# Performance work log

Measured on AMD Instinct MI355X. Metric: run time of the kernel, lower is better.

## Reference

```python
import jax, jax.numpy as jnp
import numpy as np

# PyTorch LSTM cell with zero initial (h, c): W_hh @ h0 == 0, and c = sigmoid(i)*tanh(g)
# since the forget-gate term f*c0 vanishes. Gate order in torch: i, f, g, o.
# b here is the combined b_ih + b_hh (identical math).

def lstm_step0(x, Wih, b):
    pre = x @ Wih.T + b                      # (N, 4H)
    i, f, g, o = jnp.split(pre, 4, axis=-1)
    c = jax.nn.sigmoid(i) * jnp.tanh(g)
    return jax.nn.sigmoid(o) * jnp.tanh(c)   # (N, H)


def setup_inputs() -> dict:
    key = jax.random.key(0)
    ks = jax.random.split(key, 13)
    num_ts, num_periods, F = 128, 256, 128
    GH, NH, NF = 512, 256, 10
    s = lambda k, shape, fan: (jax.random.normal(k, shape, jnp.float32) / np.sqrt(fan))
    return {
        "X": jax.random.normal(ks[0], (num_ts, num_periods, F), jnp.float32),
        "g_Wih0": s(ks[1], (4 * GH, F), F),
        "g_b0": s(ks[2], (4 * GH,), GH),
        "g_Wih1": s(ks[3], (4 * GH, GH), GH),
        "g_b1": s(ks[4], (4 * GH,), GH),
        "aff_W": s(ks[5], (NF, GH), GH),
        "aff_b": s(ks[6], (NF,), GH),
        "n_Wih0": s(ks[7], (4 * NH, F), F),
        "n_b0": s(ks[8], (4 * NH,), NH),
        "n_Wih1": s(ks[9], (4 * NH, NH), NH),
        "n_b1": s(ks[10], (4 * NH,), NH),
        "noise_W": s(ks[11], (1, NH), NH),
        "noise_b": s(ks[12], (1,), NH),
    }


def reference(X, g_Wih0, g_b0, g_Wih1, g_b1, aff_W, aff_b,
              n_Wih0, n_b0, n_Wih1, n_b1, noise_W, noise_b):
    num_ts, num_periods, num_feats = X.shape
    x = X.reshape(-1, num_feats)             # (num_ts*num_periods, F)

    # Global factor branch: 2-layer LSTM single step from zero state
    hg = lstm_step0(lstm_step0(x, g_Wih0, g_b0), g_Wih1, g_b1)
    hg = jax.nn.relu(hg)
    mus = (hg @ aff_W.T + aff_b).sum(axis=-1).reshape(num_ts, num_periods)

    # Noise branch: 2-layer LSTM single step from zero state
    hn = lstm_step0(lstm_step0(x, n_Wih0, n_b0), n_Wih1, n_b1)
    hn = jax.nn.relu(hn)
    sigmas = jax.nn.softplus(hn @ noise_W.T + noise_b)  # log(1+exp(.)), stable
    sigmas = sigmas.reshape(num_ts, num_periods) + 1e-6
    return mus, sigmas
```

## Files before the change

### kernel.cpp

```cpp
#include <hip/hip_runtime.h>
#include <hip/hip_bf16.h>
#include <hip/hip_fp16.h>

typedef _Float16 h8_t __attribute__((ext_vector_type(8)));
typedef _Float16 h4_t __attribute__((ext_vector_type(4)));
typedef float f4_t __attribute__((ext_vector_type(4)));

#define M_ROWS 32768

__device__ __forceinline__ void gload_lds16(const void* g, void* l) {
  __builtin_amdgcn_global_load_lds((const __attribute__((address_space(1))) void*)g,
                                   (__attribute__((address_space(3))) void*)l, 16, 0, 0);
}

__device__ __forceinline__ float sigmoid_f(float x) { return 1.f / (1.f + __expf(-x)); }
__device__ __forceinline__ float tanh_f(float x) { return 1.f - 2.f / (__expf(2.f * x) + 1.f); }

struct GArgs {
  const _Float16* A;
  const _Float16* W;
  const float* bias;
  _Float16* Hout;
  const float* rvec;
  float* partial;
};

__global__ void prep_all(const float* __restrict__ X, const float* __restrict__ gW0,
                         const float* __restrict__ gW1, const float* __restrict__ nW0,
                         const float* __restrict__ nW1, const float* __restrict__ aff_W,
                         const float* __restrict__ aff_b,
                         _Float16* __restrict__ Xh, _Float16* __restrict__ Wg0,
                         _Float16* __restrict__ Wg1, _Float16* __restrict__ Wn0,
                         _Float16* __restrict__ Wn1,
                         float* __restrict__ pg, float* __restrict__ pn,
                         float* __restrict__ wsum) {
  int b = blockIdx.x;
  const float* s; _Float16* d; int base;
  if (b < 4096)      { s = X;   d = Xh;  base = b; }
  else if (b < 4352) { s = gW0; d = Wg0; base = b - 4096; }
  else if (b < 5376) { s = gW1; d = Wg1; base = b - 4352; }
  else if (b < 5504) { s = nW0; d = Wn0; base = b - 5376; }
  else if (b < 5760) { s = nW1; d = Wn1; base = b - 5504; }
  else if (b < 5888) {
    int i = (b - 5760) * 256 + threadIdx.x;
    pg[i] = 0.f; pn[i] = 0.f;
    return;
  } else {
    int j = (b - 5888) * 256 + threadIdx.x;
    float sum = 0.f;
#pragma unroll
    for (int r = 0; r < 10; ++r) sum += aff_W[r * 512 + j];
    wsum[j] = sum;
    if (j == 0) {
      float bs = 0.f;
#pragma unroll
      for (int r = 0; r < 10; ++r) bs += aff_b[r];
      wsum[512] = bs;
    }
    return;
  }
  int i4 = (base * 256 + threadIdx.x) * 4;
  float4 v = *(const float4*)(s + i4);
  h4_t o;
  o[0] = (_Float16)v.x; o[1] = (_Float16)v.y; o[2] = (_Float16)v.z; o[3] = (_Float16)v.w;
  *(h4_t*)(d + i4) = o;
}

template <int K_DIM, int H_DIM, bool FUSE>
__device__ __forceinline__ void gemm_body(const GArgs& ga, int h0,
                                          _Float16* As, _Float16* Bs) {
  const int tid = threadIdx.x;
  const int wid = tid >> 6;
  const int lane = tid & 63;
  const int wave_m = wid >> 1;
  const int wave_h = wid & 1;
  const int q = lane >> 4;
  const int tcol = lane & 15;
  const int m0 = blockIdx.x * 128;

  constexpr int NT = K_DIM / 64;
  constexpr int A_BYTES = 128 * 64 * 2;
  constexpr int B_BYTES = 3 * 64 * 64 * 2;
  constexpr int A_ELEMS = 128 * 64;
  constexpr int B_ELEMS = 3 * 64 * 64;

  const _Float16* aptr[4]; int aoff[4];
#pragma unroll
  for (int c = 0; c < 4; ++c) {
    int o = ((wid * 4 + c) << 10) + (lane << 4);
    int row = o >> 7, pch = (o >> 4) & 7;
    int lch = pch ^ (row & 7);
    aptr[c] = ga.A + (size_t)(m0 + row) * K_DIM + lch * 8;
    aoff[c] = o;
  }
  const _Float16* bptr[6]; int boff[6];
#pragma unroll
  for (int c = 0; c < 6; ++c) {
    int o = ((wid * 6 + c) << 10) + (lane << 4);
    int pan = o >> 13;
    int row = (o >> 7) & 63, pch = (o >> 4) & 7;
    int lch = pch ^ (row & 7);
    int gbase = (pan == 0 ? 0 : (pan == 1 ? 2 * H_DIM : 3 * H_DIM)) + h0 + row;
    bptr[c] = ga.W + (size_t)gbase * K_DIM + lch * 8;
    boff[c] = o;
  }
  int a_rd[2][4];
#pragma unroll
  for (int ks = 0; ks < 2; ++ks)
#pragma unroll
    for (int mi = 0; mi < 4; ++mi) {
      int r = wave_m * 64 + mi * 16 + tcol;
      int c = ks * 4 + q;
      a_rd[ks][mi] = r * 64 + (c ^ (r & 7)) * 8;
    }
  int b_rd[2][2];
#pragma unroll
  for (int ks = 0; ks < 2; ++ks)
#pragma unroll
    for (int ni = 0; ni < 2; ++ni) {
      int j = wave_h * 32 + ni * 16 + tcol;
      int c = ks * 4 + q;
      b_rd[ks][ni] = j * 64 + (c ^ (j & 7)) * 8;
    }

  f4_t acc[3][4][2];
#pragma unroll
  for (int p = 0; p < 3; ++p)
#pragma unroll
    for (int mi = 0; mi < 4; ++mi)
#pragma unroll
      for (int ni = 0; ni < 2; ++ni) acc[p][mi][ni] = (f4_t){0.f, 0.f, 0.f, 0.f};

#pragma unroll
  for (int c = 0; c < 4; ++c) gload_lds16(aptr[c], (char*)As + aoff[c]);
#pragma unroll
  for (int c = 0; c < 6; ++c) gload_lds16(bptr[c], (char*)Bs + boff[c]);
#pragma unroll
  for (int c = 0; c < 4; ++c) aptr[c] += 64;
#pragma unroll
  for (int c = 0; c < 6; ++c) bptr[c] += 64;
  __syncthreads();

#pragma unroll
  for (int kk = 0; kk < NT; ++kk) {
    const int cur = kk & 1;
    const int nxt = cur ^ 1;
    if (kk < NT - 1) {
#pragma unroll
      for (int c = 0; c < 4; ++c) gload_lds16(aptr[c], (char*)As + nxt * A_BYTES + aoff[c]);
#pragma unroll
      for (int c = 0; c < 6; ++c) gload_lds16(bptr[c], (char*)Bs + nxt * B_BYTES + boff[c]);
#pragma unroll
      for (int c = 0; c < 4; ++c) aptr[c] += 64;
#pragma unroll
      for (int c = 0; c < 6; ++c) bptr[c] += 64;
    }

#pragma unroll
    for (int ks = 0; ks < 2; ++ks) {
      h8_t af[4];
#pragma unroll
      for (int mi = 0; mi < 4; ++mi) af[mi] = *(const h8_t*)&As[cur * A_ELEMS + a_rd[ks][mi]];
#pragma unroll
      for (int p = 0; p < 3; ++p) {
#pragma unroll
        for (int ni = 0; ni < 2; ++ni) {
          h8_t bf = *(const h8_t*)&Bs[cur * B_ELEMS + p * 4096 + b_rd[ks][ni]];
#pragma unroll
          for (int mi = 0; mi < 4; ++mi)
            acc[p][mi][ni] = __builtin_amdgcn_mfma_f32_16x16x32_f16(af[mi], bf, acc[p][mi][ni], 0, 0, 0);
        }
      }
    }
    if (kk < NT - 1) __syncthreads();
  }

  const int mrow0 = m0 + wave_m * 64;
  const int jcol0 = h0 + wave_h * 32;

  if constexpr (!FUSE) {
#pragma unroll
    for (int ni = 0; ni < 2; ++ni) {
      int j = jcol0 + ni * 16 + tcol;
      float bi = ga.bias[j];
      float bg = ga.bias[2 * H_DIM + j];
      float bo = ga.bias[3 * H_DIM + j];
#pragma unroll
      for (int mi = 0; mi < 4; ++mi)
#pragma unroll
        for (int r = 0; r < 4; ++r) {
          float pi = acc[0][mi][ni][r] + bi;
          float pgt = acc[1][mi][ni][r] + bg;
          float po = acc[2][mi][ni][r] + bo;
          float cc = sigmoid_f(pi) * tanh_f(pgt);
          float hh = sigmoid_f(po) * tanh_f(cc);
          int m = mrow0 + mi * 16 + q * 4 + r;
          ga.Hout[(size_t)m * H_DIM + j] = (_Float16)hh;
        }
    }
  } else {
    float rsum[4][4];
#pragma unroll
    for (int mi = 0; mi < 4; ++mi)
#pragma unroll
      for (int r = 0; r < 4; ++r) rsum[mi][r] = 0.f;
#pragma unroll
    for (int ni = 0; ni < 2; ++ni) {
      int j = jcol0 + ni * 16 + tcol;
      float bi = ga.bias[j];
      float bg = ga.bias[2 * H_DIM + j];
      float bo = ga.bias[3 * H_DIM + j];
      float rv = ga.rvec[j];
#pragma unroll
      for (int mi = 0; mi < 4; ++mi)
#pragma unroll
        for (int r = 0; r < 4; ++r) {
          float pi = acc[0][mi][ni][r] + bi;
          float pgt = acc[1][mi][ni][r] + bg;
          float po = acc[2][mi][ni][r] + bo;
          float cc = sigmoid_f(pi) * tanh_f(pgt);
          float hh = sigmoid_f(po) * tanh_f(cc);
          hh = fmaxf(hh, 0.f);
          rsum[mi][r] += hh * rv;
        }
    }
#pragma unroll
    for (int mi = 0; mi < 4; ++mi)
#pragma unroll
      for (int r = 0; r < 4; ++r) {
        float v = rsum[mi][r];
        v += __shfl_xor(v, 1);
        v += __shfl_xor(v, 2);
        v += __shfl_xor(v, 4);
        v += __shfl_xor(v, 8);
        if (tcol == 0) atomicAdd(&ga.partial[mrow0 + mi * 16 + q * 4 + r], v);
      }
  }
}

__global__ __launch_bounds__(256, 2) void layer1_fused(GArgs g, GArgs n) {
  __shared__ __align__(16) _Float16 As[2 * 128 * 64];
  __shared__ __align__(16) _Float16 Bs[2 * 3 * 64 * 64];
  int y = blockIdx.y;
  if (y < 8) gemm_body<128, 512, false>(g, y * 64, As, Bs);
  else       gemm_body<128, 256, false>(n, (y - 8) * 64, As, Bs);
}

__global__ __launch_bounds__(256, 2) void layer2_fused(GArgs g, GArgs n) {
  __shared__ __align__(16) _Float16 As[2 * 128 * 64];
  __shared__ __align__(16) _Float16 Bs[2 * 3 * 64 * 64];
  int y = blockIdx.y;
  if (y < 8) gemm_body<512, 512, true>(g, y * 64, As, Bs);
  else       gemm_body<256, 256, true>(n, (y - 8) * 64, As, Bs);
}

__global__ void finalize(const float* __restrict__ pg, const float* __restrict__ pn,
                         const float* __restrict__ wsum, const float* __restrict__ noise_b,
                         float* __restrict__ out) {
  int i = blockIdx.x * blockDim.x + threadIdx.x;
  out[i] = pg[i] + wsum[512];
  float x = pn[i] + noise_b[0];
  float sp = fmaxf(x, 0.f) + log1pf(expf(-fabsf(x)));
  out[M_ROWS + i] = sp + 1e-6f;
}

extern "C" void kernel_launch(void* const* d_in, const int* in_sizes, int n_in,
                              void* d_out, int out_size, void* d_ws, size_t ws_size,
                              hipStream_t stream) {
  const float* X       = (const float*)d_in[0];
  const float* g_Wih0  = (const float*)d_in[1];
  const float* g_b0    = (const float*)d_in[2];
  const float* g_Wih1  = (const float*)d_in[3];
  const float* g_b1    = (const float*)d_in[4];
  const float* aff_W   = (const float*)d_in[5];
  const float* aff_b   = (const float*)d_in[6];
  const float* n_Wih0  = (const float*)d_in[7];
  const float* n_b0    = (const float*)d_in[8];
  const float* n_Wih1  = (const float*)d_in[9];
  const float* n_b1    = (const float*)d_in[10];
  const float* noise_W = (const float*)d_in[11];
  const float* noise_b = (const float*)d_in[12];
  float* out = (float*)d_out;

  char* w = (char*)d_ws;
  _Float16* Xh  = (_Float16*)w; w += (size_t)M_ROWS * 128 * 2;
  _Float16* Wg0 = (_Float16*)w; w += 2048 * 128 * 2;
  _Float16* Wg1 = (_Float16*)w; w += 2048 * 512 * 2;
  _Float16* Wn0 = (_Float16*)w; w += 1024 * 128 * 2;
  _Float16* Wn1 = (_Float16*)w; w += 1024 * 256 * 2;
  _Float16* h1g = (_Float16*)w; w += (size_t)M_ROWS * 512 * 2;
  _Float16* h1n = (_Float16*)w; w += (size_t)M_ROWS * 256 * 2;
  float* pg   = (float*)w; w += (size_t)M_ROWS * 4;
  float* pn   = (float*)w; w += (size_t)M_ROWS * 4;
  float* wsum = (float*)w; w += 4096;

  prep_all<<<5890, 256, 0, stream>>>(X, g_Wih0, g_Wih1, n_Wih0, n_Wih1, aff_W, aff_b,
                                     Xh, Wg0, Wg1, Wn0, Wn1, pg, pn, wsum);

  GArgs l1g = {Xh, Wg0, g_b0, h1g, nullptr, nullptr};
  GArgs l1n = {Xh, Wn0, n_b0, h1n, nullptr, nullptr};
  layer1_fused<<<dim3(M_ROWS / 128, 12), 256, 0, stream>>>(l1g, l1n);

  GArgs l2g = {h1g, Wg1, g_b1, nullptr, wsum, pg};
  GArgs l2n = {h1n, Wn1, n_b1, nullptr, noise_W, pn};
  layer2_fused<<<dim3(M_ROWS / 128, 12), 256, 0, stream>>>(l2g, l2n);

  finalize<<<M_ROWS / 256, 256, 0, stream>>>(pg, pn, wsum, noise_b, out);
}
```

Measured before the change: 311.2 us.

## Use partial vmcnt waits with raw barriers and swizzle block order for L2 reuse

Replaces the __syncthreads calls in the double-buffered GEMM loop with explicit s_waitcnt vmcnt(10) and a raw s_barrier. Each iteration then waits only for the current tile's async global-to-LDS loads, while the next tile's loads stay in flight. It also remaps the linear block index so that consecutive blocks cover all 12 H-tiles of the same 128-row M-tile, spread across 8 groups, to improve L2 reuse of A rows. The risk is correctness: the hand-counted vmcnt must match the number of outstanding loads issued per thread, and the swizzle assumes a 256x12 grid.

```diff
diff --git a/kernel.cpp b/kernel.cpp
--- a/kernel.cpp
+++ b/kernel.cpp
@@ -67,7 +67,7 @@
 }
 
 template <int K_DIM, int H_DIM, bool FUSE>
-__device__ __forceinline__ void gemm_body(const GArgs& ga, int h0,
+__device__ __forceinline__ void gemm_body(const GArgs& ga, int h0, int m0,
                                           _Float16* As, _Float16* Bs) {
   const int tid = threadIdx.x;
   const int wid = tid >> 6;
@@ -76,7 +76,6 @@
   const int wave_h = wid & 1;
   const int q = lane >> 4;
   const int tcol = lane & 15;
-  const int m0 = blockIdx.x * 128;
 
   constexpr int NT = K_DIM / 64;
   constexpr int A_BYTES = 128 * 64 * 2;
@@ -139,7 +138,6 @@
   for (int c = 0; c < 4; ++c) aptr[c] += 64;
 #pragma unroll
   for (int c = 0; c < 6; ++c) bptr[c] += 64;
-  __syncthreads();
 
 #pragma unroll
   for (int kk = 0; kk < NT; ++kk) {
@@ -154,7 +152,12 @@
       for (int c = 0; c < 4; ++c) aptr[c] += 64;
 #pragma unroll
       for (int c = 0; c < 6; ++c) bptr[c] += 64;
-    }
+      asm volatile("s_waitcnt vmcnt(10)" ::: "memory");
+    } else {
+      asm volatile("s_waitcnt vmcnt(0)" ::: "memory");
+    }
+    __builtin_amdgcn_s_barrier();
+    asm volatile("" ::: "memory");
 
 #pragma unroll
     for (int ks = 0; ks < 2; ++ks) {
@@ -172,7 +175,8 @@
         }
       }
     }
-    if (kk < NT - 1) __syncthreads();
+    asm volatile("" ::: "memory");
+    if (kk < NT - 1) __builtin_amdgcn_s_barrier();
   }
 
   const int mrow0 = m0 + wave_m * 64;
@@ -238,20 +242,28 @@
   }
 }
 
+__device__ __forceinline__ void swizzle_xy(int& x, int& y) {
+  int lin = blockIdx.y * gridDim.x + blockIdx.x;
+  int c = lin & 7;
+  int r = lin >> 3;
+  y = r % 12;
+  x = c * 32 + r / 12;
+}
+
 __global__ __launch_bounds__(256, 2) void layer1_fused(GArgs g, GArgs n) {
   __shared__ __align__(16) _Float16 As[2 * 128 * 64];
   __shared__ __align__(16) _Float16 Bs[2 * 3 * 64 * 64];
-  int y = blockIdx.y;
-  if (y < 8) gemm_body<128, 512, false>(g, y * 64, As, Bs);
-  else       gemm_body<128, 256, false>(n, (y - 8) * 64, As, Bs);
+  int x, y; swizzle_xy(x, y);
+  if (y < 8) gemm_body<128, 512, false>(g, y * 64, x * 128, As, Bs);
+  else       gemm_body<128, 256, false>(n, (y - 8) * 64, x * 128, As, Bs);
 }
 
 __global__ __launch_bounds__(256, 2) void layer2_fused(GArgs g, GArgs n) {
   __shared__ __align__(16) _Float16 As[2 * 128 * 64];
   __shared__ __align__(16) _Float16 Bs[2 * 3 * 64 * 64];
-  int y = blockIdx.y;
-  if (y < 8) gemm_body<512, 512, true>(g, y * 64, As, Bs);
-  else       gemm_body<256, 256, true>(n, (y - 8) * 64, As, Bs);
+  int x, y; swizzle_xy(x, y);
+  if (y < 8) gemm_body<512, 512, true>(g, y * 64, x * 128, As, Bs);
+  else       gemm_body<256, 256, true>(n, (y - 8) * 64, x * 128, As, Bs);
 }
 
 __global__ void finalize(const float* __restrict__ pg, const float* __restrict__ pn,
```

Result: faster. 274.3 us (-11.9%).
